# Performance work log

Hardware: AMD Instinct MI355X
Metric: run time of the kernel (lower is better)

Reference implementation:

```python
import jax, jax.numpy as jnp
import numpy as np

N_LAYER = 6
N_EMBD = 768
N_HEAD = 12
BLOCK_SIZE = 256
SEG = 10
B = 2
T_SEG = 256  # t (== block_size here)


def setup_inputs() -> dict:
    key = jax.random.key(0)
    ks = iter(jax.random.split(key, 64))
    C, L = N_EMBD, N_LAYER
    d = {}
    for name in ['idx_up', 'idx_down', 'idx_lhand', 'idx_rhand', 'idx_transl',
                 'cond_music', 'cond_up', 'cond_down', 'cond_lhand', 'cond_rhand']:
        d[name] = jax.random.normal(next(ks), (B, T_SEG, C), dtype=jnp.float32)
    d['pos_emb'] = 0.02 * jax.random.normal(next(ks), (1, BLOCK_SIZE * SEG, C), dtype=jnp.float32)
    d['ln1_w'] = jnp.ones((L, C), jnp.float32)
    d['ln1_b'] = jnp.zeros((L, C), jnp.float32)
    d['ln2_w'] = jnp.ones((L, C), jnp.float32)
    d['ln2_b'] = jnp.zeros((L, C), jnp.float32)
    for nm in ['Wq', 'Wk', 'Wv', 'Wp']:
        d[nm] = 0.02 * jax.random.normal(next(ks), (L, C, C), dtype=jnp.float32)
    for nm in ['bq', 'bk', 'bv', 'bp']:
        d[nm] = jnp.zeros((L, C), jnp.float32)
    d['W1'] = 0.02 * jax.random.normal(next(ks), (L, 4 * C, C), dtype=jnp.float32)
    d['b1'] = jnp.zeros((L, 4 * C), jnp.float32)
    d['W2'] = 0.02 * jax.random.normal(next(ks), (L, C, 4 * C), dtype=jnp.float32)
    d['b2'] = jnp.zeros((L, C), jnp.float32)
    return d


def _layer_norm(x, w, b, eps=1e-5):
    mu = jnp.mean(x, axis=-1, keepdims=True)
    var = jnp.mean((x - mu) ** 2, axis=-1, keepdims=True)
    return (x - mu) * jax.lax.rsqrt(var + eps) * w + b


def _block(x, mask, ln1_w, ln1_b, Wq, bq, Wk, bk, Wv, bv, Wp, bp, ln2_w, ln2_b, W1, b1, W2, b2):
    Bq, T, C = x.shape
    H, hd = N_HEAD, C // N_HEAD
    h = _layer_norm(x, ln1_w, ln1_b)
    q = (h @ Wq.T + bq).reshape(Bq, T, H, hd).transpose(0, 2, 1, 3)  # [B,H,T,hd]
    k = (h @ Wk.T + bk).reshape(Bq, T, H, hd).transpose(0, 2, 1, 3)
    v = (h @ Wv.T + bv).reshape(Bq, T, H, hd).transpose(0, 2, 1, 3)
    att = jnp.einsum('bhqd,bhkd->bhqk', q, k) * (1.0 / np.sqrt(hd))
    att = jnp.where(mask == 0, -jnp.inf, att)
    att = jax.nn.softmax(att, axis=-1)
    y = jnp.einsum('bhqk,bhkd->bhqd', att, v).transpose(0, 2, 1, 3).reshape(Bq, T, C)
    x = x + (y @ Wp.T + bp)
    h2 = _layer_norm(x, ln2_w, ln2_b)
    h2 = jax.nn.gelu(h2 @ W1.T + b1, approximate=False) @ W2.T + b2
    return x + h2


def reference(idx_up, idx_down, idx_lhand, idx_rhand, idx_transl,
              cond_music, cond_up, cond_down, cond_lhand, cond_rhand,
              pos_emb, ln1_w, ln1_b, ln2_w, ln2_b,
              Wq, Wk, Wv, Wp, bq, bk, bv, bp, W1, b1, W2, b2):
    t = idx_up.shape[1]
    Tb = BLOCK_SIZE
    tok = jnp.concatenate([cond_music, cond_up, cond_down, cond_lhand, cond_rhand,
                           idx_up, idx_down, idx_lhand, idx_rhand, idx_transl], axis=1)
    pos = jnp.concatenate([pos_emb[:, s * Tb:s * Tb + t, :] for s in range(SEG)], axis=1)
    x = tok + pos
    # tiled block-causal mask: tril(t,t) repeated 10x10
    tri = jnp.tril(jnp.ones((t, t), jnp.float32))
    mask = jnp.tile(tri, (SEG, SEG))  # [T, T]
    for li in range(N_LAYER):
        x = _block(x, mask,
                   ln1_w[li], ln1_b[li], Wq[li], bq[li], Wk[li], bk[li],
                   Wv[li], bv[li], Wp[li], bp[li], ln2_w[li], ln2_b[li],
                   W1[li], b1[li], W2[li], b2[li])
    return x
```

## Files before the change

kernel.cpp:

```cpp
#include <hip/hip_runtime.h>
#include <hip/hip_bf16.h>
#include <stdint.h>
#include <stddef.h>

typedef unsigned short u16;
typedef __attribute__((ext_vector_type(8))) short bf16x8;
typedef __attribute__((ext_vector_type(4))) float f32x4;
typedef __attribute__((ext_vector_type(4))) unsigned short u16x4;

#define TC 768
#define TT 2560
#define NB 2
#define NM (NB * TT)
#define NH 12
#define HD 64
#define NL 6
#define LDQ 1536

static __device__ __forceinline__ u16 f2bf(float f) {
  return __builtin_bit_cast(u16, __float2bfloat16(f));
}

static __device__ __forceinline__ float fast_exp2(float x) {
#if __has_builtin(__builtin_amdgcn_exp2f)
  return __builtin_amdgcn_exp2f(x);
#else
  return exp2f(x);
#endif
}

static __device__ __forceinline__ void gload16(const void* g, void* l) {
  __builtin_amdgcn_global_load_lds((const __attribute__((address_space(1))) void*)g,
                                   (__attribute__((address_space(3))) void*)l, 16, 0, 0);
}

__global__ __launch_bounds__(256) void embed_kernel(
    const float* __restrict__ cm, const float* __restrict__ cu, const float* __restrict__ cd,
    const float* __restrict__ cl, const float* __restrict__ cr,
    const float* __restrict__ iu, const float* __restrict__ id_, const float* __restrict__ il,
    const float* __restrict__ ir, const float* __restrict__ it,
    const float* __restrict__ pos, float* __restrict__ x)
{
  int v = blockIdx.x * 256 + threadIdx.x;
  const int NV = NM * TC / 4;
  if (v >= NV) return;
  int e = v * 4;
  int b = e / (TT * TC);
  int rem = e - b * (TT * TC);
  int tpos = rem / TC;
  int c = rem - tpos * TC;
  int s = tpos >> 8;
  int tt = tpos & 255;
  const float* src;
  switch (s) {
    case 0: src = cm; break; case 1: src = cu; break; case 2: src = cd; break;
    case 3: src = cl; break; case 4: src = cr; break; case 5: src = iu; break;
    case 6: src = id_; break; case 7: src = il; break; case 8: src = ir; break;
    default: src = it; break;
  }
  f32x4 a = *(const f32x4*)&src[(size_t)(b * 256 + tt) * TC + c];
  f32x4 p = *(const f32x4*)&pos[(size_t)tpos * TC + c];
  *(f32x4*)&x[e] = a + p;
}

__global__ __launch_bounds__(256) void conv_all_kernel(
    const float* __restrict__ Wq, const float* __restrict__ Wk, const float* __restrict__ Wv,
    const float* __restrict__ Wp, const float* __restrict__ W1, const float* __restrict__ W2,
    u16* __restrict__ wqkv, u16* __restrict__ wp, u16* __restrict__ w1, u16* __restrict__ w2)
{
  const int SQ = 768 * 768;
  int v = blockIdx.x * 256 + threadIdx.x;
  int e = v * 4;
  const float* src; u16* dst;
  if (e < 3 * SQ) {
    int wsel = e / SQ; int le = e - wsel * SQ;
    src = (wsel == 0 ? Wq : wsel == 1 ? Wk : Wv) + le;
    dst = wqkv + e;
  } else if (e < 4 * SQ) {
    src = Wp + (e - 3 * SQ); dst = wp + (e - 3 * SQ);
  } else if (e < 8 * SQ) {
    src = W1 + (e - 4 * SQ); dst = w1 + (e - 4 * SQ);
  } else {
    src = W2 + (e - 8 * SQ); dst = w2 + (e - 8 * SQ);
  }
  f32x4 f = *(const f32x4*)src;
  u16x4 r;
  r[0] = f2bf(f[0]); r[1] = f2bf(f[1]); r[2] = f2bf(f[2]); r[3] = f2bf(f[3]);
  *(u16x4*)dst = r;
}

__global__ __launch_bounds__(192) void ln_kernel(
    const float* __restrict__ x, const float* __restrict__ w, const float* __restrict__ bb,
    u16* __restrict__ out)
{
  int row = blockIdx.x;
  int tid = threadIdx.x;
  f32x4 v = *(const f32x4*)&x[(size_t)row * TC + tid * 4];
  float s = v[0] + v[1] + v[2] + v[3];
  float ss = v[0] * v[0] + v[1] * v[1] + v[2] * v[2] + v[3] * v[3];
  #pragma unroll
  for (int m = 1; m < 64; m <<= 1) { s += __shfl_xor(s, m, 64); ss += __shfl_xor(ss, m, 64); }
  __shared__ float red[6];
  int wave = tid >> 6, lane = tid & 63;
  if (lane == 0) { red[wave] = s; red[3 + wave] = ss; }
  __syncthreads();
  s = red[0] + red[1] + red[2];
  ss = red[3] + red[4] + red[5];
  const float inv = 1.0f / 768.0f;
  float mu = s * inv;
  float var = ss * inv - mu * mu;
  float rs = rsqrtf(var + 1e-5f);
  f32x4 wv = *(const f32x4*)&w[tid * 4];
  f32x4 bv = *(const f32x4*)&bb[tid * 4];
  u16x4 o4;
  #pragma unroll
  for (int j = 0; j < 4; ++j) o4[j] = f2bf((v[j] - mu) * rs * wv[j] + bv[j]);
  *(u16x4*)&out[(size_t)row * TC + tid * 4] = o4;
}

template<int EPI>
__global__ __launch_bounds__(512, 4) void gemm_kernel(
    const u16* __restrict__ A, const u16* __restrict__ Bw,
    const float* __restrict__ b0, const float* __restrict__ b1, const float* __restrict__ b2,
    u16* __restrict__ outb, u16* __restrict__ vTout, int K, int N)
{
  __shared__ __align__(16) u16 As[2][128 * 64];
  __shared__ __align__(16) u16 Bs[2][128 * 64];
  const int bm = blockIdx.x, bn = blockIdx.y;
  const int tid = threadIdx.x;
  const int wave = tid >> 6;
  const int lane = tid & 63;
  const int wr = wave >> 2, wc = wave & 3;
  const int l15 = lane & 15, l16 = lane >> 4;

  f32x4 acc[4][2];
  #pragma unroll
  for (int m = 0; m < 4; ++m)
    #pragma unroll
    for (int n = 0; n < 2; ++n) acc[m][n] = f32x4{0.f, 0.f, 0.f, 0.f};

  const u16* gA0 = A + (size_t)(bm * 128) * K;
  const u16* gB0 = Bw + (size_t)(bn * 128) * K;

  #define GSTAGE(BUF, KT)                                                        \
    {                                                                            \
      const u16* ga = gA0 + (size_t)(KT) * 64;                                   \
      const u16* gb = gB0 + (size_t)(KT) * 64;                                   \
      _Pragma("unroll")                                                          \
      for (int i = 0; i < 2; ++i) {                                              \
        int s = i * 512 + tid; int row = s >> 3; int c = (s & 7) ^ (row & 7);    \
        gload16(ga + (size_t)row * K + c * 8, &As[BUF][s * 8]);                  \
      }                                                                          \
      _Pragma("unroll")                                                          \
      for (int i = 0; i < 2; ++i) {                                              \
        int s = i * 512 + tid; int row = s >> 3; int c = (s & 7) ^ (row & 7);    \
        gload16(gb + (size_t)row * K + c * 8, &Bs[BUF][s * 8]);                  \
      }                                                                          \
    }

  const int nkt = K >> 6;
  GSTAGE(0, 0)

  for (int kt = 0; kt < nkt; ++kt) {
    const int cb = kt & 1;
    if (kt + 1 < nkt) {
      GSTAGE(cb ^ 1, kt + 1)
      asm volatile("s_waitcnt vmcnt(4)" ::: "memory");
    } else {
      asm volatile("s_waitcnt vmcnt(0)" ::: "memory");
    }
    __builtin_amdgcn_s_barrier();
    __builtin_amdgcn_sched_barrier(0);
    #pragma unroll
    for (int kk = 0; kk < 2; ++kk) {
      bf16x8 aF[4], bF[2];
      #pragma unroll
      for (int m = 0; m < 4; ++m) {
        int row = wr * 64 + m * 16 + l15;
        aF[m] = *(const bf16x8*)&As[cb][row * 64 + (((kk * 4 + l16) ^ (row & 7)) * 8)];
      }
      #pragma unroll
      for (int n = 0; n < 2; ++n) {
        int row = wc * 32 + n * 16 + l15;
        bF[n] = *(const bf16x8*)&Bs[cb][row * 64 + (((kk * 4 + l16) ^ (row & 7)) * 8)];
      }
      __builtin_amdgcn_s_setprio(1);
      #pragma unroll
      for (int m = 0; m < 4; ++m)
        #pragma unroll
        for (int n = 0; n < 2; ++n)
          acc[m][n] = __builtin_amdgcn_mfma_f32_16x16x32_bf16(aF[m], bF[n], acc[m][n], 0, 0, 0);
      __builtin_amdgcn_s_setprio(0);
    }
    __builtin_amdgcn_sched_barrier(0);
    __builtin_amdgcn_s_barrier();
  }
  #undef GSTAGE

  #pragma unroll
  for (int m = 0; m < 4; ++m) {
    int row = bm * 128 + wr * 64 + m * 16 + l16 * 4;
    #pragma unroll
    for (int n = 0; n < 2; ++n) {
      int col = bn * 128 + wc * 32 + n * 16 + l15;
      if (EPI == 0) {
        float bv = (col < 768) ? b0[col] : (col < 1536 ? b1[col - 768] : b2[col - 1536]);
        if (col < 1536) {
          float sc = (col < 768) ? 0.180336880f : 1.0f;
          #pragma unroll
          for (int r = 0; r < 4; ++r)
            outb[(size_t)(row + r) * LDQ + col] = f2bf((acc[m][n][r] + bv) * sc);
        } else {
          int cc = col - 1536, hh = cc >> 6, dd = cc & 63;
          int bb2 = (row >= TT) ? 1 : 0;
          int t = row - bb2 * TT;
          int k6 = t & 63;
          int c6 = k6 >> 4, g6 = (k6 >> 2) & 3;
          int tp = (t & ~63) | ((c6 & 2) << 4) | (g6 << 3) | ((c6 & 1) << 2);
          u16x4 pk;
          #pragma unroll
          for (int r = 0; r < 4; ++r) pk[r] = f2bf(acc[m][n][r] + bv);
          *(u16x4*)&vTout[((size_t)(bb2 * NH + hh) * HD + dd) * TT + tp] = pk;
        }
      } else {
        float bv = b0[col];
        #pragma unroll
        for (int r = 0; r < 4; ++r) {
          float v = acc[m][n][r] + bv;
          float g = 0.5f * v * (1.0f + erff(v * 0.70710678118654752f));
          outb[(size_t)(row + r) * N + col] = f2bf(g);
        }
      }
    }
  }
}

__global__ __launch_bounds__(512, 4) void gemm64_kernel(
    const u16* __restrict__ A, const u16* __restrict__ Bw,
    const float* __restrict__ b0, float* __restrict__ resid, int K, int N)
{
  __shared__ __align__(16) u16 As[2][64 * 64];
  __shared__ __align__(16) u16 Bs[2][128 * 64];
  const int bm = blockIdx.x, bn = blockIdx.y;
  const int tid = threadIdx.x;
  const int wave = tid >> 6;
  const int lane = tid & 63;
  const int wr = wave >> 2, wc = wave & 3;
  const int l15 = lane & 15, l16 = lane >> 4;

  f32x4 acc[2][2];
  #pragma unroll
  for (int m = 0; m < 2; ++m)
    #pragma unroll
    for (int n = 0; n < 2; ++n) acc[m][n] = f32x4{0.f, 0.f, 0.f, 0.f};

  const u16* gA0 = A + (size_t)(bm * 64) * K;
  const u16* gB0 = Bw + (size_t)(bn * 128) * K;

  #define GSTAGE64(BUF, KT)                                                      \
    {                                                                            \
      const u16* ga = gA0 + (size_t)(KT) * 64;                                   \
      const u16* gb = gB0 + (size_t)(KT) * 64;                                   \
      {                                                                          \
        int s = tid; int row = s >> 3; int c = (s & 7) ^ (row & 7);              \
        gload16(ga + (size_t)row * K + c * 8, &As[BUF][s * 8]);                  \
      }                                                                          \
      _Pragma("unroll")                                                          \
      for (int i = 0; i < 2; ++i) {                                              \
        int s = i * 512 + tid; int row = s >> 3; int c = (s & 7) ^ (row & 7);    \
        gload16(gb + (size_t)row * K + c * 8, &Bs[BUF][s * 8]);                  \
      }                                                                          \
    }

  const int nkt = K >> 6;
  GSTAGE64(0, 0)

  for (int kt = 0; kt < nkt; ++kt) {
    const int cb = kt & 1;
    if (kt + 1 < nkt) {
      GSTAGE64(cb ^ 1, kt + 1)
      asm volatile("s_waitcnt vmcnt(3)" ::: "memory");
    } else {
      asm volatile("s_waitcnt vmcnt(0)" ::: "memory");
    }
    __builtin_amdgcn_s_barrier();
    __builtin_amdgcn_sched_barrier(0);
    #pragma unroll
    for (int kk = 0; kk < 2; ++kk) {
      bf16x8 aF[2], bF[2];
      #pragma unroll
      for (int m = 0; m < 2; ++m) {
        int row = wr * 32 + m * 16 + l15;
        aF[m] = *(const bf16x8*)&As[cb][row * 64 + (((kk * 4 + l16) ^ (row & 7)) * 8)];
      }
      #pragma unroll
      for (int n = 0; n < 2; ++n) {
        int row = wc * 32 + n * 16 + l15;
        bF[n] = *(const bf16x8*)&Bs[cb][row * 64 + (((kk * 4 + l16) ^ (row & 7)) * 8)];
      }
      __builtin_amdgcn_s_setprio(1);
      #pragma unroll
      for (int m = 0; m < 2; ++m)
        #pragma unroll
        for (int n = 0; n < 2; ++n)
          acc[m][n] = __builtin_amdgcn_mfma_f32_16x16x32_bf16(aF[m], bF[n], acc[m][n], 0, 0, 0);
      __builtin_amdgcn_s_setprio(0);
    }
    __builtin_amdgcn_sched_barrier(0);
    __builtin_amdgcn_s_barrier();
  }
  #undef GSTAGE64

  #pragma unroll
  for (int m = 0; m < 2; ++m) {
    int row = bm * 64 + wr * 32 + m * 16 + l16 * 4;
    #pragma unroll
    for (int n = 0; n < 2; ++n) {
      int col = bn * 128 + wc * 32 + n * 16 + l15;
      float bv = b0[col];
      #pragma unroll
      for (int r = 0; r < 4; ++r)
        resid[(size_t)(row + r) * N + col] += acc[m][n][r] + bv;
    }
  }
}

__global__ __launch_bounds__(256, 8) void attn_kernel(
    const u16* __restrict__ qk, const u16* __restrict__ vT, u16* __restrict__ yb)
{
  __shared__ __align__(16) u16 Ks[2][64 * 64];
  __shared__ __align__(16) u16 Vs[2][64 * 64];
  const int tid = threadIdx.x;
  const int wave = tid >> 6, lane = tid & 63;
  const int l15 = lane & 15, l16 = lane >> 4;
  const int idx = blockIdx.x;
  const int g = idx / 24;
  const int bh = idx - g * 24;
  const int jd = 3 - (g / 10);
  const int qt = (g - (3 - jd) * 10) * 4 + jd;
  const int b = bh / NH, h = bh - (bh / NH) * NH;
  const int q0 = qt * 64 + wave * 16;
  const int qloc = wave * 16 + l15;

  const u16* qb = qk + (size_t)b * TT * LDQ + h * HD;
  const u16* kb = qb + 768;
  const u16* vt = vT + (size_t)(b * NH + h) * HD * TT;

  bf16x8 qB0 = *(const bf16x8*)&qb[(size_t)(q0 + l15) * LDQ + l16 * 8];
  bf16x8 qB1 = *(const bf16x8*)&qb[(size_t)(q0 + l15) * LDQ + 32 + l16 * 8];

  bf16x8 ones;
  #pragma unroll
  for (int i = 0; i < 8; ++i) ones[i] = (short)0x3F80;

  f32x4 o[4];
  #pragma unroll
  for (int n = 0; n < 4; ++n) o[n] = f32x4{0.f, 0.f, 0.f, 0.f};
  f32x4 osum = f32x4{0.f, 0.f, 0.f, 0.f};

  const int sl0 = tid >> 3;
  const int sp  = tid & 7;

  #define STAGE(BUF, K0)                                                            \
    {                                                                               \
      _Pragma("unroll")                                                             \
      for (int rr = 0; rr < 2; ++rr) {                                              \
        int row = rr * 32 + sl0;                                                    \
        int sl = sp ^ (row & 7);                                                    \
        int slot = row * 8 + sp;                                                    \
        gload16(&kb[(size_t)((K0) + row) * LDQ + sl * 8], &Ks[BUF][slot * 8]);      \
        gload16(&vt[(size_t)row * TT + (K0) + sl * 8], &Vs[BUF][slot * 8]);         \
      }                                                                             \
    }

  STAGE(0, 0)
  int cur = 0;

  union U { u16x4 h[2]; bf16x8 v; };

  for (int ks = 0; ks < 10; ++ks) {
    for (int j = 0; j <= jd; ++j) {
      const bool last = (ks == 9) && (j == jd);
      if (!last) {
        int nk0 = (j < jd) ? ks * 256 + (j + 1) * 64 : (ks + 1) * 256;
        STAGE(cur ^ 1, nk0)
        asm volatile("s_waitcnt vmcnt(4)" ::: "memory");
      } else {
        asm volatile("s_waitcnt vmcnt(0)" ::: "memory");
      }
      __builtin_amdgcn_s_barrier();
      __builtin_amdgcn_sched_barrier(0);

      f32x4 s[4];
      __builtin_amdgcn_s_setprio(1);
      #pragma unroll
      for (int c = 0; c < 4; ++c) {
        int row = c * 16 + l15, sw = row & 7;
        bf16x8 k0f = *(const bf16x8*)&Ks[cur][row * 64 + ((l16 ^ sw) * 8)];
        bf16x8 k1f = *(const bf16x8*)&Ks[cur][row * 64 + (((4 + l16) ^ sw) * 8)];
        f32x4 z = __builtin_amdgcn_mfma_f32_16x16x32_bf16(k0f, qB0, f32x4{0.f,0.f,0.f,0.f}, 0, 0, 0);
        s[c] = __builtin_amdgcn_mfma_f32_16x16x32_bf16(k1f, qB1, z, 0, 0, 0);
      }
      __builtin_amdgcn_s_setprio(0);

      if (j == jd) {
        #pragma unroll
        for (int c = 0; c < 4; ++c)
          #pragma unroll
          for (int r = 0; r < 4; ++r)
            if (c * 16 + l16 * 4 + r > qloc) s[c][r] = -1e30f;
      }

      u16x4 wcp[4];
      #pragma unroll
      for (int c = 0; c < 4; ++c)
        #pragma unroll
        for (int r = 0; r < 4; ++r)
          wcp[c][r] = f2bf(fast_exp2(s[c][r]));
      U p0, p1;
      p0.h[0] = wcp[0]; p0.h[1] = wcp[1];
      p1.h[0] = wcp[2]; p1.h[1] = wcp[3];
      __builtin_amdgcn_s_setprio(1);
      osum = __builtin_amdgcn_mfma_f32_16x16x32_bf16(ones, p0.v, osum, 0, 0, 0);
      osum = __builtin_amdgcn_mfma_f32_16x16x32_bf16(ones, p1.v, osum, 0, 0, 0);
      #pragma unroll
      for (int mt = 0; mt < 4; ++mt) {
        int row = mt * 16 + l15, sw = row & 7;
        const u16* vrow = &Vs[cur][row * 64];
        bf16x8 v0 = *(const bf16x8*)&vrow[(l16 ^ sw) * 8];
        bf16x8 v1 = *(const bf16x8*)&vrow[((4 + l16) ^ sw) * 8];
        o[mt] = __builtin_amdgcn_mfma_f32_16x16x32_bf16(v0, p0.v, o[mt], 0, 0, 0);
        o[mt] = __builtin_amdgcn_mfma_f32_16x16x32_bf16(v1, p1.v, o[mt], 0, 0, 0);
      }
      __builtin_amdgcn_s_setprio(0);
      __builtin_amdgcn_sched_barrier(0);
      __builtin_amdgcn_s_barrier();
      cur ^= 1;
    }
  }
  #undef STAGE

  float invl = 1.0f / osum[0];
  u16* yr = &yb[(size_t)(b * TT + q0 + l15) * TC + h * HD];
  #pragma unroll
  for (int mt = 0; mt < 4; ++mt) {
    u16x4 pk;
    pk[0] = f2bf(o[mt][0] * invl); pk[1] = f2bf(o[mt][1] * invl);
    pk[2] = f2bf(o[mt][2] * invl); pk[3] = f2bf(o[mt][3] * invl);
    *(u16x4*)&yr[mt * 16 + l16 * 4] = pk;
  }
}

extern "C" void kernel_launch(void* const* d_in, const int* in_sizes, int n_in,
                              void* d_out, int out_size, void* d_ws, size_t ws_size,
                              hipStream_t stream)
{
  (void)in_sizes; (void)n_in; (void)out_size; (void)ws_size;
  const float* IU = (const float*)d_in[0];
  const float* ID = (const float*)d_in[1];
  const float* IL = (const float*)d_in[2];
  const float* IR = (const float*)d_in[3];
  const float* IT = (const float*)d_in[4];
  const float* CM = (const float*)d_in[5];
  const float* CU = (const float*)d_in[6];
  const float* CD = (const float*)d_in[7];
  const float* CL = (const float*)d_in[8];
  const float* CR = (const float*)d_in[9];
  const float* POS = (const float*)d_in[10];
  const float* LN1W = (const float*)d_in[11];
  const float* LN1B = (const float*)d_in[12];
  const float* LN2W = (const float*)d_in[13];
  const float* LN2B = (const float*)d_in[14];
  const float* WQ = (const float*)d_in[15];
  const float* WK = (const float*)d_in[16];
  const float* WV = (const float*)d_in[17];
  const float* WP = (const float*)d_in[18];
  const float* BQ = (const float*)d_in[19];
  const float* BK = (const float*)d_in[20];
  const float* BV = (const float*)d_in[21];
  const float* BP = (const float*)d_in[22];
  const float* W1 = (const float*)d_in[23];
  const float* B1 = (const float*)d_in[24];
  const float* W2 = (const float*)d_in[25];
  const float* B2 = (const float*)d_in[26];

  float* x = (float*)d_out;
  char* ws = (char*)d_ws;
  u16* ws_wqkv = (u16*)(ws + 0);
  u16* ws_wp   = (u16*)(ws + 3538944);
  u16* ws_w1   = (u16*)(ws + 4718592);
  u16* ws_w2   = (u16*)(ws + 9437184);
  u16* ws_h    = (u16*)(ws + 14155776);
  u16* ws_qkv  = (u16*)(ws + 22020096);
  u16* ws_vt   = (u16*)(ws + 37748736);
  u16* ws_y    = (u16*)(ws + 45613056);
  u16* ws_g    = ws_qkv;

  embed_kernel<<<(NM * TC / 4) / 256, 256, 0, stream>>>(CM, CU, CD, CL, CR, IU, ID, IL, IR, IT, POS, x);

  const int SQ = 768 * 768;
  const int W1SL = 3072 * 768;
  for (int li = 0; li < NL; ++li) {
    conv_all_kernel<<<6912, 256, 0, stream>>>(
        WQ + (size_t)li * SQ, WK + (size_t)li * SQ, WV + (size_t)li * SQ,
        WP + (size_t)li * SQ, W1 + (size_t)li * W1SL, W2 + (size_t)li * W1SL,
        ws_wqkv, ws_wp, ws_w1, ws_w2);

    ln_kernel<<<NM, 192, 0, stream>>>(x, LN1W + li * TC, LN1B + li * TC, ws_h);
    gemm_kernel<0><<<dim3(NM / 128, 2304 / 128), 512, 0, stream>>>(
        ws_h, ws_wqkv, BQ + li * TC, BK + li * TC, BV + li * TC, ws_qkv, ws_vt, 768, 2304);
    attn_kernel<<<dim3(40 * 24), 256, 0, stream>>>(ws_qkv, ws_vt, ws_y);
    gemm64_kernel<<<dim3(NM / 64, 768 / 128), 512, 0, stream>>>(
        ws_y, ws_wp, BP + li * TC, x, 768, 768);
    ln_kernel<<<NM, 192, 0, stream>>>(x, LN2W + li * TC, LN2B + li * TC, ws_h);
    gemm_kernel<1><<<dim3(NM / 128, 3072 / 128), 512, 0, stream>>>(
        ws_h, ws_w1, B1 + (size_t)li * 3072, nullptr, nullptr, ws_g, nullptr, 768, 3072);
    gemm64_kernel<<<dim3(NM / 64, 768 / 128), 512, 0, stream>>>(
        ws_g, ws_w2, B2 + li * TC, x, 3072, 768);
  }
}
```

Measured before the change: 1.095 ms.

## Switch QKV and FC1 GEMMs to 32x32x16 MFMA with 4-wave 64x64 warp tiles

Rewrites the 128x128-tile GEMM to use 256 threads (4 waves), each computing a 64x64 subtile with 32x32x16 bf16 MFMA instructions instead of 8 waves using 16x16x32. Larger per-wave tiles raise register-level reuse and cut LDS fragment reads per FLOP, and the larger MFMA shape has better throughput. The epilogue is remapped to the 32x32 accumulator layout, including the V-transpose scatter. Fewer waves per block may reduce latency hiding, and higher register pressure limits occupancy.

```diff
diff --git a/kernel.cpp b/kernel.cpp
--- a/kernel.cpp
+++ b/kernel.cpp
@@ -6,6 +6,7 @@
 typedef unsigned short u16;
 typedef __attribute__((ext_vector_type(8))) short bf16x8;
 typedef __attribute__((ext_vector_type(4))) float f32x4;
+typedef __attribute__((ext_vector_type(16))) float f32x16;
 typedef __attribute__((ext_vector_type(4))) unsigned short u16x4;
 
 #define TC 768
@@ -119,7 +120,7 @@
 }
 
 template<int EPI>
-__global__ __launch_bounds__(512, 4) void gemm_kernel(
+__global__ __launch_bounds__(256, 2) void gemm32_kernel(
     const u16* __restrict__ A, const u16* __restrict__ Bw,
     const float* __restrict__ b0, const float* __restrict__ b1, const float* __restrict__ b2,
     u16* __restrict__ outb, u16* __restrict__ vTout, int K, int N)
@@ -130,105 +131,114 @@
   const int tid = threadIdx.x;
   const int wave = tid >> 6;
   const int lane = tid & 63;
-  const int wr = wave >> 2, wc = wave & 3;
-  const int l15 = lane & 15, l16 = lane >> 4;
-
-  f32x4 acc[4][2];
-  #pragma unroll
-  for (int m = 0; m < 4; ++m)
+  const int wr = wave >> 1, wc = wave & 1;
+  const int l31 = lane & 31, lh = lane >> 5;
+
+  f32x16 acc[2][2];
+  #pragma unroll
+  for (int mi = 0; mi < 2; ++mi)
     #pragma unroll
-    for (int n = 0; n < 2; ++n) acc[m][n] = f32x4{0.f, 0.f, 0.f, 0.f};
+    for (int ni = 0; ni < 2; ++ni)
+      #pragma unroll
+      for (int r = 0; r < 16; ++r) acc[mi][ni][r] = 0.f;
 
   const u16* gA0 = A + (size_t)(bm * 128) * K;
   const u16* gB0 = Bw + (size_t)(bn * 128) * K;
 
-  #define GSTAGE(BUF, KT)                                                        \
+  #define GSTAGE32(BUF, KT)                                                      \
     {                                                                            \
       const u16* ga = gA0 + (size_t)(KT) * 64;                                   \
       const u16* gb = gB0 + (size_t)(KT) * 64;                                   \
       _Pragma("unroll")                                                          \
-      for (int i = 0; i < 2; ++i) {                                              \
-        int s = i * 512 + tid; int row = s >> 3; int c = (s & 7) ^ (row & 7);    \
+      for (int i = 0; i < 4; ++i) {                                              \
+        int s = i * 256 + tid; int row = s >> 3; int c = (s & 7) ^ (row & 7);    \
         gload16(ga + (size_t)row * K + c * 8, &As[BUF][s * 8]);                  \
       }                                                                          \
       _Pragma("unroll")                                                          \
-      for (int i = 0; i < 2; ++i) {                                              \
-        int s = i * 512 + tid; int row = s >> 3; int c = (s & 7) ^ (row & 7);    \
+      for (int i = 0; i < 4; ++i) {                                              \
+        int s = i * 256 + tid; int row = s >> 3; int c = (s & 7) ^ (row & 7);    \
         gload16(gb + (size_t)row * K + c * 8, &Bs[BUF][s * 8]);                  \
       }                                                                          \
     }
 
   const int nkt = K >> 6;
-  GSTAGE(0, 0)
+  GSTAGE32(0, 0)
 
   for (int kt = 0; kt < nkt; ++kt) {
     const int cb = kt & 1;
     if (kt + 1 < nkt) {
-      GSTAGE(cb ^ 1, kt + 1)
-      asm volatile("s_waitcnt vmcnt(4)" ::: "memory");
+      GSTAGE32(cb ^ 1, kt + 1)
+      asm volatile("s_waitcnt vmcnt(8)" ::: "memory");
     } else {
       asm volatile("s_waitcnt vmcnt(0)" ::: "memory");
     }
     __builtin_amdgcn_s_barrier();
     __builtin_amdgcn_sched_barrier(0);
     #pragma unroll
-    for (int kk = 0; kk < 2; ++kk) {
-      bf16x8 aF[4], bF[2];
-      #pragma unroll
-      for (int m = 0; m < 4; ++m) {
-        int row = wr * 64 + m * 16 + l15;
-        aF[m] = *(const bf16x8*)&As[cb][row * 64 + (((kk * 4 + l16) ^ (row & 7)) * 8)];
-      }
-      #pragma unroll
-      for (int n = 0; n < 2; ++n) {
-        int row = wc * 32 + n * 16 + l15;
-        bF[n] = *(const bf16x8*)&Bs[cb][row * 64 + (((kk * 4 + l16) ^ (row & 7)) * 8)];
+    for (int ks = 0; ks < 4; ++ks) {
+      bf16x8 aF[2], bF[2];
+      #pragma unroll
+      for (int mi = 0; mi < 2; ++mi) {
+        int row = wr * 64 + mi * 32 + l31;
+        aF[mi] = *(const bf16x8*)&As[cb][row * 64 + (((ks * 2 + lh) ^ (row & 7)) * 8)];
+      }
+      #pragma unroll
+      for (int ni = 0; ni < 2; ++ni) {
+        int row = wc * 64 + ni * 32 + l31;
+        bF[ni] = *(const bf16x8*)&Bs[cb][row * 64 + (((ks * 2 + lh) ^ (row & 7)) * 8)];
       }
       __builtin_amdgcn_s_setprio(1);
       #pragma unroll
-      for (int m = 0; m < 4; ++m)
+      for (int mi = 0; mi < 2; ++mi)
         #pragma unroll
-        for (int n = 0; n < 2; ++n)
-          acc[m][n] = __builtin_amdgcn_mfma_f32_16x16x32_bf16(aF[m], bF[n], acc[m][n], 0, 0, 0);
+        for (int ni = 0; ni < 2; ++ni)
+          acc[mi][ni] = __builtin_amdgcn_mfma_f32_32x32x16_bf16(aF[mi], bF[ni], acc[mi][ni], 0, 0, 0);
       __builtin_amdgcn_s_setprio(0);
     }
     __builtin_amdgcn_sched_barrier(0);
     __builtin_amdgcn_s_barrier();
   }
-  #undef GSTAGE
-
-  #pragma unroll
-  for (int m = 0; m < 4; ++m) {
-    int row = bm * 128 + wr * 64 + m * 16 + l16 * 4;
+  #undef GSTAGE32
+
+  #pragma unroll
+  for (int mi = 0; mi < 2; ++mi) {
     #pragma unroll
-    for (int n = 0; n < 2; ++n) {
-      int col = bn * 128 + wc * 32 + n * 16 + l15;
+    for (int ni = 0; ni < 2; ++ni) {
+      int col = bn * 128 + wc * 64 + ni * 32 + l31;
       if (EPI == 0) {
         float bv = (col < 768) ? b0[col] : (col < 1536 ? b1[col - 768] : b2[col - 1536]);
-        if (col < 1536) {
-          float sc = (col < 768) ? 0.180336880f : 1.0f;
-          #pragma unroll
-          for (int r = 0; r < 4; ++r)
-            outb[(size_t)(row + r) * LDQ + col] = f2bf((acc[m][n][r] + bv) * sc);
-        } else {
-          int cc = col - 1536, hh = cc >> 6, dd = cc & 63;
-          int bb2 = (row >= TT) ? 1 : 0;
-          int t = row - bb2 * TT;
-          int k6 = t & 63;
-          int c6 = k6 >> 4, g6 = (k6 >> 2) & 3;
-          int tp = (t & ~63) | ((c6 & 2) << 4) | (g6 << 3) | ((c6 & 1) << 2);
-          u16x4 pk;
-          #pragma unroll
-          for (int r = 0; r < 4; ++r) pk[r] = f2bf(acc[m][n][r] + bv);
-          *(u16x4*)&vTout[((size_t)(bb2 * NH + hh) * HD + dd) * TT + tp] = pk;
+        float sc = (col < 768) ? 0.180336880f : 1.0f;
+        #pragma unroll
+        for (int g = 0; g < 4; ++g) {
+          int row0 = bm * 128 + wr * 64 + mi * 32 + g * 8 + lh * 4;
+          if (col < 1536) {
+            #pragma unroll
+            for (int e = 0; e < 4; ++e)
+              outb[(size_t)(row0 + e) * LDQ + col] = f2bf((acc[mi][ni][g * 4 + e] + bv) * sc);
+          } else {
+            int cc = col - 1536, hh = cc >> 6, dd = cc & 63;
+            int bb2 = (row0 >= TT) ? 1 : 0;
+            int t = row0 - bb2 * TT;
+            int k6 = t & 63;
+            int c6 = k6 >> 4, g6 = (k6 >> 2) & 3;
+            int tp = (t & ~63) | ((c6 & 2) << 4) | (g6 << 3) | ((c6 & 1) << 2);
+            u16x4 pk;
+            #pragma unroll
+            for (int e = 0; e < 4; ++e) pk[e] = f2bf(acc[mi][ni][g * 4 + e] + bv);
+            *(u16x4*)&vTout[((size_t)(bb2 * NH + hh) * HD + dd) * TT + tp] = pk;
+          }
         }
       } else {
         float bv = b0[col];
         #pragma unroll
-        for (int r = 0; r < 4; ++r) {
-          float v = acc[m][n][r] + bv;
-          float g = 0.5f * v * (1.0f + erff(v * 0.70710678118654752f));
-          outb[(size_t)(row + r) * N + col] = f2bf(g);
+        for (int g = 0; g < 4; ++g) {
+          int row0 = bm * 128 + wr * 64 + mi * 32 + g * 8 + lh * 4;
+          #pragma unroll
+          for (int e = 0; e < 4; ++e) {
+            float v = acc[mi][ni][g * 4 + e] + bv;
+            float gl = 0.5f * v * (1.0f + erff(v * 0.70710678118654752f));
+            outb[(size_t)(row0 + e) * N + col] = f2bf(gl);
+          }
         }
       }
     }
@@ -507,13 +517,13 @@
         ws_wqkv, ws_wp, ws_w1, ws_w2);
 
     ln_kernel<<<NM, 192, 0, stream>>>(x, LN1W + li * TC, LN1B + li * TC, ws_h);
-    gemm_kernel<0><<<dim3(NM / 128, 2304 / 128), 512, 0, stream>>>(
+    gemm32_kernel<0><<<dim3(NM / 128, 2304 / 128), 256, 0, stream>>>(
         ws_h, ws_wqkv, BQ + li * TC, BK + li * TC, BV + li * TC, ws_qkv, ws_vt, 768, 2304);
     attn_kernel<<<dim3(40 * 24), 256, 0, stream>>>(ws_qkv, ws_vt, ws_y);
     gemm64_kernel<<<dim3(NM / 64, 768 / 128), 512, 0, stream>>>(
         ws_y, ws_wp, BP + li * TC, x, 768, 768);
     ln_kernel<<<NM, 192, 0, stream>>>(x, LN2W + li * TC, LN2B + li * TC, ws_h);
-    gemm_kernel<1><<<dim3(NM / 128, 3072 / 128), 512, 0, stream>>>(
+    gemm32_kernel<1><<<dim3(NM / 128, 3072 / 128), 256, 0, stream>>>(
         ws_h, ws_w1, B1 + (size_t)li * 3072, nullptr, nullptr, ws_g, nullptr, 768, 3072);
     gemm64_kernel<<<dim3(NM / 64, 768 / 128), 512, 0, stream>>>(
         ws_g, ws_w2, B2 + li * TC, x, 3072, 768);
```

Result: slower. 1.194 ms (+9.0%).
